# Kernel tuning notes

Measured on AMD Instinct MI355X. Metric: run time of the kernel, lower is better.

The kernel has to match this reference:

```python
import jax, jax.numpy as jnp
import numpy as np

H, I, E, S, K = 768, 3072, 16, 2, 2
SCALE = 1.0  # routed_scaling_factor


def setup_inputs() -> dict:
    key = jax.random.key(0)
    ks = jax.random.split(key, 8)
    sd = 0.02
    return {
        "hidden_states": jax.random.normal(ks[0], (2, 1024, H), jnp.float32),
        "gate_w": jax.random.normal(ks[1], (E, H), jnp.float32) * sd,   # router nn.Linear(H,E).weight
        "shared_wg": jax.random.normal(ks[2], (S, H, I), jnp.float32) * sd,
        "shared_wu": jax.random.normal(ks[3], (S, H, I), jnp.float32) * sd,
        "shared_wd": jax.random.normal(ks[4], (S, I, H), jnp.float32) * sd,
        "wg": jax.random.normal(ks[5], (E, H, I), jnp.float32) * sd,
        "wu": jax.random.normal(ks[6], (E, H, I), jnp.float32) * sd,
        "wd": jax.random.normal(ks[7], (E, I, H), jnp.float32) * sd,
    }


def reference(hidden_states, gate_w, shared_wg, shared_wu, shared_wd, wg, wu, wd):
    B, T, _ = hidden_states.shape
    x = hidden_states.reshape(-1, H)                       # [N, H], N = B*T
    N = x.shape[0]

    # ---- shared experts: always-on, averaged ----
    g = jnp.einsum('nh,shi->sni', x, shared_wg)
    u = jnp.einsum('nh,shi->sni', x, shared_wu)
    shared_out = jnp.einsum('sni,sih->snh', jax.nn.silu(g) * u, shared_wd).mean(axis=0)

    # ---- router: softmax scores, top-k, renormalize, scale ----
    router_logits = x @ gate_w.T                           # [N, E]
    routing_weights = jax.nn.softmax(router_logits, axis=-1)
    topk_w, topk_idx = jax.lax.top_k(routing_weights, K)   # [N, K]
    topk_w = topk_w / (topk_w.sum(axis=-1, keepdims=True) + 1e-8)
    topk_w = topk_w * SCALE

    # combine weights: [N, E], zero for non-selected experts (duplicates summed,
    # matching the torch per-token weight-sum semantics)
    combine = jnp.zeros((N, E), x.dtype).at[jnp.arange(N)[:, None], topk_idx].add(topk_w)

    # ---- routed experts: weighted combine (w=0 for unselected -> same math) ----
    ge = jnp.einsum('nh,ehi->eni', x, wg)                  # [E, N, I]
    ue = jnp.einsum('nh,ehi->eni', x, wu)
    ye = jnp.einsum('eni,eih->enh', jax.nn.silu(ge) * ue, wd)  # [E, N, H]
    routed_out = jnp.einsum('ne,enh->nh', combine, ye)

    return (shared_out + routed_out).reshape(B, T, H)
```

## Files before the change

### kernel.cpp

```cpp
#include <hip/hip_runtime.h>
#include <hip/hip_bf16.h>

#define H 768
#define I_DIM 3072
#define NEXP 16
#define TOPK 2

typedef __bf16 bf16;
typedef __bf16 bf16x8 __attribute__((ext_vector_type(8)));
typedef float f32x4 __attribute__((ext_vector_type(4)));

__device__ __forceinline__ int swizzle_mtile(int bx, int gx) {
    int per = gx >> 3;
    if ((per << 3) != gx) return bx;
    return (bx & 7) * per + (bx >> 3);
}

__global__ void cvt_x_kernel(const float* __restrict__ x, bf16* __restrict__ xb, int n) {
    int i = (blockIdx.x * blockDim.x + threadIdx.x) * 8;
    if (i >= n) return;
    f32x4 v0 = *(const f32x4*)(x + i);
    f32x4 v1 = *(const f32x4*)(x + i + 4);
    bf16x8 p;
#pragma unroll
    for (int j = 0; j < 4; j++) { p[j] = (bf16)v0[j]; p[4 + j] = (bf16)v1[j]; }
    *(bf16x8*)(xb + i) = p;
}

__global__ void router_kernel(const float* __restrict__ x, const float* __restrict__ gw,
                              int* __restrict__ tk_e, float* __restrict__ tk_w,
                              int* __restrict__ counts, int N) {
    int wave = threadIdx.x >> 6;
    int lane = threadIdx.x & 63;
    int t = blockIdx.x * 4 + wave;
    if (t >= N) return;
    const float* xr = x + (size_t)t * H;
    float acc[NEXP];
#pragma unroll
    for (int e = 0; e < NEXP; e++) acc[e] = 0.f;
    for (int h0 = 0; h0 < H; h0 += 64) {
        float xv = xr[h0 + lane];
#pragma unroll
        for (int e = 0; e < NEXP; e++) acc[e] += xv * gw[e * H + h0 + lane];
    }
#pragma unroll
    for (int e = 0; e < NEXP; e++) {
#pragma unroll
        for (int off = 32; off > 0; off >>= 1) acc[e] += __shfl_xor(acc[e], off);
    }
    if (lane == 0) {
        float m = acc[0];
#pragma unroll
        for (int e = 1; e < NEXP; e++) m = fmaxf(m, acc[e]);
        float p[NEXP]; float z = 0.f;
#pragma unroll
        for (int e = 0; e < NEXP; e++) { p[e] = expf(acc[e] - m); z += p[e]; }
        float inv = 1.f / z;
#pragma unroll
        for (int e = 0; e < NEXP; e++) p[e] *= inv;
        int i0 = 0; float v0 = p[0];
#pragma unroll
        for (int e = 1; e < NEXP; e++) if (p[e] > v0) { v0 = p[e]; i0 = e; }
        int i1 = -1; float v1 = -1.f;
#pragma unroll
        for (int e = 0; e < NEXP; e++) if (e != i0 && p[e] > v1) { v1 = p[e]; i1 = e; }
        float s = 1.f / (v0 + v1 + 1e-8f);
        tk_e[t * 2 + 0] = i0; tk_w[t * 2 + 0] = v0 * s;
        tk_e[t * 2 + 1] = i1; tk_w[t * 2 + 1] = v1 * s;
        atomicAdd(&counts[i0], 1);
        atomicAdd(&counts[i1], 1);
    }
}

__global__ void scan_fill_kernel(const int* __restrict__ counts, int* __restrict__ cursors,
                                 int* __restrict__ pad_off, int* __restrict__ rows_token,
                                 float* __restrict__ rows_weight, int N) {
    __shared__ int s_total;
    if (threadIdx.x == 0) {
        int off = 0;
        for (int e = 0; e < NEXP; e++) {
            pad_off[e] = off;
            cursors[e] = off;
            off += (counts[e] + 127) & ~127;
        }
        pad_off[NEXP] = off;
        s_total = off;
    }
    __syncthreads();
    int total = s_total;
    for (int r = threadIdx.x; r < 2 * N; r += blockDim.x) {
        rows_token[r] = r & (N - 1);
        rows_weight[r] = 0.5f;
    }
    for (int r = threadIdx.x; r < total; r += blockDim.x) {
        rows_token[2 * N + r] = 0;
        rows_weight[2 * N + r] = 0.f;
    }
}

__global__ void scatter_kernel(const int* __restrict__ tk_e, const float* __restrict__ tk_w,
                               int* __restrict__ cursors, int* __restrict__ rows_token,
                               float* __restrict__ rows_weight, int N) {
    int i = blockIdx.x * blockDim.x + threadIdx.x;
    if (i >= N * TOPK) return;
    int e = tk_e[i];
    int pos = atomicAdd(&cursors[e], 1);
    rows_token[2 * N + pos] = i >> 1;
    rows_weight[2 * N + pos] = tk_w[i];
}

__global__ __launch_bounds__(256) void phaseA_kernel(
        const bf16* __restrict__ xb, const float* __restrict__ swg, const float* __restrict__ swu,
        const float* __restrict__ wg, const float* __restrict__ wu,
        const int* __restrict__ pad_off, const int* __restrict__ rows_token,
        bf16* __restrict__ P, int N, int ic0, int ichunk) {
    int mtile = swizzle_mtile(blockIdx.x, gridDim.x);
    int ntile = blockIdx.y;
    int sh_tiles = (2 * N) / 128;
    int rowbase; const float* gptr; const float* uptr;
    if (mtile < sh_tiles) {
        rowbase = mtile * 128;
        int s = rowbase / N;
        gptr = swg + (size_t)s * H * I_DIM;
        uptr = swu + (size_t)s * H * I_DIM;
    } else {
        int rm = (mtile - sh_tiles) * 128;
        if (rm >= pad_off[NEXP]) return;
        int e = NEXP - 1;
        for (int q = 0; q < NEXP; q++) { if (rm < pad_off[q + 1]) { e = q; break; } }
        rowbase = 2 * N + rm;
        gptr = wg + (size_t)e * H * I_DIM;
        uptr = wu + (size_t)e * H * I_DIM;
    }
    int icol0 = ic0 + ntile * 64;
    int pcol0 = ntile * 64;

    __shared__ bf16 As[2][128][40];
    __shared__ bf16 Bgs[2][64][40];
    __shared__ bf16 Bus[2][64][40];
    __shared__ int sTok[128];

    int tid = threadIdx.x;
    if (tid < 128) sTok[tid] = rows_token[rowbase + tid];
    __syncthreads();

    f32x4 accG[4][2], accU[4][2];
#pragma unroll
    for (int i = 0; i < 4; i++)
#pragma unroll
        for (int j = 0; j < 2; j++) {
            accG[i][j] = (f32x4){0.f, 0.f, 0.f, 0.f};
            accU[i][j] = (f32x4){0.f, 0.f, 0.f, 0.f};
        }

    int ar = tid >> 1, ah = tid & 1;
    const bf16* arow = xb + (size_t)sTok[ar] * H + ah * 16;
    int bn = tid & 63, bkq = tid >> 6;
    const float* gbase = gptr + icol0 + bn;
    const float* ubase = uptr + icol0 + bn;

    int lane = tid & 63, w = tid >> 6;
    int wm = (w & 1) * 64, wn = (w >> 1) * 32;
    int fr = lane & 15, fq = (lane >> 4) * 8;

    bf16x8 rA0, rA1;
    float gv[8], uv[8];

#define PA_LOADK(kk)                                                          \
    {                                                                         \
        rA0 = *(const bf16x8*)(arow + (kk));                                  \
        rA1 = *(const bf16x8*)(arow + (kk) + 8);                              \
        _Pragma("unroll")                                                     \
        for (int j = 0; j < 8; j++) {                                         \
            gv[j] = gbase[(size_t)((kk) + bkq * 8 + j) * I_DIM];              \
            uv[j] = ubase[(size_t)((kk) + bkq * 8 + j) * I_DIM];              \
        }                                                                     \
    }
#define PA_STORE(buf)                                                         \
    {                                                                         \
        *(bf16x8*)&As[buf][ar][ah * 16] = rA0;                                \
        *(bf16x8*)&As[buf][ar][ah * 16 + 8] = rA1;                            \
        bf16x8 pg, pu;                                                        \
        _Pragma("unroll")                                                     \
        for (int j = 0; j < 8; j++) { pg[j] = (bf16)gv[j]; pu[j] = (bf16)uv[j]; } \
        *(bf16x8*)&Bgs[buf][bn][bkq * 8] = pg;                                \
        *(bf16x8*)&Bus[buf][bn][bkq * 8] = pu;                                \
    }

    PA_LOADK(0);
    PA_STORE(0);
    __syncthreads();

#pragma unroll
    for (int kb = 0; kb < 24; kb++) {
        if (kb < 23) PA_LOADK((kb + 1) * 32);
        int cur = kb & 1;
        bf16x8 a[4], bg[2], bu[2];
#pragma unroll
        for (int mi = 0; mi < 4; mi++) a[mi] = *(const bf16x8*)&As[cur][wm + mi * 16 + fr][fq];
#pragma unroll
        for (int ni = 0; ni < 2; ni++) {
            bg[ni] = *(const bf16x8*)&Bgs[cur][wn + ni * 16 + fr][fq];
            bu[ni] = *(const bf16x8*)&Bus[cur][wn + ni * 16 + fr][fq];
        }
#pragma unroll
        for (int mi = 0; mi < 4; mi++)
#pragma unroll
            for (int ni = 0; ni < 2; ni++) {
                accG[mi][ni] = __builtin_amdgcn_mfma_f32_16x16x32_bf16(a[mi], bg[ni], accG[mi][ni], 0, 0, 0);
                accU[mi][ni] = __builtin_amdgcn_mfma_f32_16x16x32_bf16(a[mi], bu[ni], accU[mi][ni], 0, 0, 0);
            }
        if (kb < 23) {
            PA_STORE(cur ^ 1);
            __syncthreads();
        }
    }

    int cq = lane >> 4;
#pragma unroll
    for (int mi = 0; mi < 4; mi++)
#pragma unroll
        for (int ni = 0; ni < 2; ni++) {
            int n = wn + ni * 16 + fr;
#pragma unroll
            for (int rr = 0; rr < 4; rr++) {
                int m = wm + mi * 16 + cq * 4 + rr;
                float g = accG[mi][ni][rr];
                float u = accU[mi][ni][rr];
                float pv = (g / (1.f + __expf(-g))) * u;
                P[(size_t)(rowbase + m) * ichunk + pcol0 + n] = (bf16)pv;
            }
        }
}

__global__ __launch_bounds__(256) void phaseB_kernel(
        const bf16* __restrict__ P, const float* __restrict__ swd, const float* __restrict__ wd,
        const int* __restrict__ pad_off, const int* __restrict__ rows_token,
        const float* __restrict__ rows_weight, float* __restrict__ out,
        int N, int ic0, int ichunk) {
    int mtile = swizzle_mtile(blockIdx.x, gridDim.x);
    int ntile = blockIdx.y;
    int sh_tiles = (2 * N) / 128;
    int rowbase; const float* dptr;
    if (mtile < sh_tiles) {
        rowbase = mtile * 128;
        int s = rowbase / N;
        dptr = swd + (size_t)s * I_DIM * H;
    } else {
        int rm = (mtile - sh_tiles) * 128;
        if (rm >= pad_off[NEXP]) return;
        int e = NEXP - 1;
        for (int q = 0; q < NEXP; q++) { if (rm < pad_off[q + 1]) { e = q; break; } }
        rowbase = 2 * N + rm;
        dptr = wd + (size_t)e * I_DIM * H;
    }
    int h0 = ntile * 128;

    __shared__ bf16 As[2][128][40];
    __shared__ bf16 Bs[2][128][40];
    __shared__ int sTok[128];
    __shared__ float sW[128];

    int tid = threadIdx.x;
    if (tid < 128) {
        sTok[tid] = rows_token[rowbase + tid];
        sW[tid] = rows_weight[rowbase + tid];
    }
    __syncthreads();

    f32x4 acc[4][4];
#pragma unroll
    for (int i = 0; i < 4; i++)
#pragma unroll
        for (int j = 0; j < 4; j++) acc[i][j] = (f32x4){0.f, 0.f, 0.f, 0.f};

    int ar = tid >> 1, ah = tid & 1;
    const bf16* arow = P + (size_t)(rowbase + ar) * ichunk + ah * 16;
    int bcol = tid & 127, bko = (tid >> 7) * 16;
    const float* dbase = dptr + (size_t)ic0 * H + h0 + bcol;

    int lane = tid & 63, w = tid >> 6;
    int wm = (w & 1) * 64, wn = (w >> 1) * 64;
    int fr = lane & 15, fq = (lane >> 4) * 8;

    bf16x8 rA0, rA1;
    float dv[16];

#define PB_LOADK(kk)                                                          \
    {                                                                         \
        rA0 = *(const bf16x8*)(arow + (kk));                                  \
        rA1 = *(const bf16x8*)(arow + (kk) + 8);                              \
        _Pragma("unroll")                                                     \
        for (int j = 0; j < 16; j++)                                          \
            dv[j] = dbase[(size_t)((kk) + bko + j) * H];                      \
    }
#define PB_STORE(buf)                                                         \
    {                                                                         \
        *(bf16x8*)&As[buf][ar][ah * 16] = rA0;                                \
        *(bf16x8*)&As[buf][ar][ah * 16 + 8] = rA1;                            \
        bf16x8 p0, p1;                                                        \
        _Pragma("unroll")                                                     \
        for (int j = 0; j < 8; j++) { p0[j] = (bf16)dv[j]; p1[j] = (bf16)dv[8 + j]; } \
        *(bf16x8*)&Bs[buf][bcol][bko] = p0;                                   \
        *(bf16x8*)&Bs[buf][bcol][bko + 8] = p1;                               \
    }

    PB_LOADK(0);
    PB_STORE(0);
    __syncthreads();

    int KB = ichunk >> 5;
    for (int kb = 0; kb < KB; kb++) {
        if (kb + 1 < KB) PB_LOADK((kb + 1) * 32);
        int cur = kb & 1;
        bf16x8 a[4], b[4];
#pragma unroll
        for (int mi = 0; mi < 4; mi++) a[mi] = *(const bf16x8*)&As[cur][wm + mi * 16 + fr][fq];
#pragma unroll
        for (int ni = 0; ni < 4; ni++) b[ni] = *(const bf16x8*)&Bs[cur][wn + ni * 16 + fr][fq];
#pragma unroll
        for (int mi = 0; mi < 4; mi++)
#pragma unroll
            for (int ni = 0; ni < 4; ni++)
                acc[mi][ni] = __builtin_amdgcn_mfma_f32_16x16x32_bf16(a[mi], b[ni], acc[mi][ni], 0, 0, 0);
        if (kb + 1 < KB) {
            PB_STORE(cur ^ 1);
            __syncthreads();
        }
    }

    int cq = lane >> 4;
#pragma unroll
    for (int mi = 0; mi < 4; mi++)
#pragma unroll
        for (int ni = 0; ni < 4; ni++) {
            int n = wn + ni * 16 + fr;
#pragma unroll
            for (int rr = 0; rr < 4; rr++) {
                int m = wm + mi * 16 + cq * 4 + rr;
                atomicAdd(&out[(size_t)sTok[m] * H + h0 + n], sW[m] * acc[mi][ni][rr]);
            }
        }
}

extern "C" void kernel_launch(void* const* d_in, const int* in_sizes, int n_in,
                              void* d_out, int out_size, void* d_ws, size_t ws_size,
                              hipStream_t stream) {
    const float* x   = (const float*)d_in[0];
    const float* gw  = (const float*)d_in[1];
    const float* swg = (const float*)d_in[2];
    const float* swu = (const float*)d_in[3];
    const float* swd = (const float*)d_in[4];
    const float* wg  = (const float*)d_in[5];
    const float* wu  = (const float*)d_in[6];
    const float* wd  = (const float*)d_in[7];
    float* out = (float*)d_out;

    int N = in_sizes[0] / H;
    int ROWCAP = 2 * N + N * TOPK + NEXP * 128;

    int* wsi = (int*)d_ws;
    int* counts     = wsi + 0;
    int* cursors    = wsi + 16;
    int* pad_off    = wsi + 32;
    int* tk_e       = wsi + 64;
    float* tk_w     = (float*)(wsi + 64 + 2 * N);
    int* rows_token = wsi + 64 + 4 * N;
    float* rows_weight = (float*)(wsi + 64 + 4 * N + ROWCAP);

    size_t xb_off = 131072;
    bf16* xb = (bf16*)((char*)d_ws + xb_off);
    size_t pbase = xb_off + (size_t)N * H * 2;

    const int cand[10] = {3072, 1536, 1024, 768, 512, 384, 256, 192, 128, 64};
    int ichunk = 64;
    for (int i = 0; i < 10; i++) {
        if (pbase + (size_t)ROWCAP * cand[i] * 2 <= ws_size) { ichunk = cand[i]; break; }
    }
    bf16* P = (bf16*)((char*)d_ws + pbase);

    hipMemsetAsync(d_out, 0, (size_t)out_size * sizeof(float), stream);
    hipMemsetAsync(d_ws, 0, 256, stream);

    cvt_x_kernel<<<(N * H) / 2048, 256, 0, stream>>>(x, xb, N * H);
    router_kernel<<<(N + 3) / 4, 256, 0, stream>>>(x, gw, tk_e, tk_w, counts, N);
    scan_fill_kernel<<<1, 256, 0, stream>>>(counts, cursors, pad_off, rows_token, rows_weight, N);
    scatter_kernel<<<(N * TOPK + 255) / 256, 256, 0, stream>>>(tk_e, tk_w, cursors, rows_token, rows_weight, N);

    int sh_tiles = (2 * N) / 128;
    int rt_tiles = (N * TOPK + NEXP * 128) / 128;
    for (int ic0 = 0; ic0 < I_DIM; ic0 += ichunk) {
        dim3 gA(sh_tiles + rt_tiles, ichunk / 64);
        phaseA_kernel<<<gA, dim3(256), 0, stream>>>(xb, swg, swu, wg, wu, pad_off, rows_token, P, N, ic0, ichunk);
        dim3 gB(sh_tiles + rt_tiles, H / 128);
        phaseB_kernel<<<gB, dim3(256), 0, stream>>>(P, swd, wd, pad_off, rows_token, rows_weight, out, N, ic0, ichunk);
    }
}
```

Before: 840.3 us.

## Pre-transpose and convert expert weights to bf16 K-major before GEMMs

Adds a transpose+convert kernel that writes all shared and routed gate/up/down weights into bf16 K-contiguous layouts in workspace, followed by new phase A/B GEMM kernels that read those bf16 transposed weights with vectorized loads. The goal is to halve weight bandwidth and avoid in-kernel fp32 conversion and strided weight access. The cost is a full pass over roughly 340MB of fp32 weights on every call plus extra workspace, with a fallback to the old path when the workspace is too small.

Result: slower. 880.8 us (+4.8%).

```diff
diff --git a/kernel.cpp b/kernel.cpp
--- a/kernel.cpp
+++ b/kernel.cpp
@@ -7,6 +7,7 @@
 #define TOPK 2
 
 typedef __bf16 bf16;
+typedef __bf16 bf16x4 __attribute__((ext_vector_type(4)));
 typedef __bf16 bf16x8 __attribute__((ext_vector_type(8)));
 typedef float f32x4 __attribute__((ext_vector_type(4)));
 
@@ -25,6 +26,32 @@
 #pragma unroll
     for (int j = 0; j < 4; j++) { p[j] = (bf16)v0[j]; p[4 + j] = (bf16)v1[j]; }
     *(bf16x8*)(xb + i) = p;
+}
+
+__global__ __launch_bounds__(256) void transpose_cvt_kernel(
+        const float* __restrict__ in, bf16* __restrict__ outp, int R, int C) {
+    __shared__ bf16 t[64][74];
+    const float* ip = in + (size_t)blockIdx.z * R * C;
+    bf16* op = outp + (size_t)blockIdx.z * R * C;
+    int c0 = blockIdx.x * 64, r0 = blockIdx.y * 64;
+    int tid = threadIdx.x;
+    int lr = tid >> 4, lc = (tid & 15) * 4;
+#pragma unroll
+    for (int p = 0; p < 4; p++) {
+        int r = p * 16 + lr;
+        f32x4 v = *(const f32x4*)(ip + (size_t)(r0 + r) * C + (c0 + lc));
+        bf16x4 b;
+#pragma unroll
+        for (int j = 0; j < 4; j++) b[j] = (bf16)v[j];
+        *(bf16x4*)&t[r][lc] = b;
+    }
+    __syncthreads();
+    int oc = tid >> 2, s = (tid & 3) * 16;
+    bf16x8 o0, o1;
+#pragma unroll
+    for (int j = 0; j < 8; j++) { o0[j] = t[s + j][oc]; o1[j] = t[s + 8 + j][oc]; }
+    *(bf16x8*)(op + (size_t)(c0 + oc) * R + (r0 + s)) = o0;
+    *(bf16x8*)(op + (size_t)(c0 + oc) * R + (r0 + s + 8)) = o1;
 }
 
 __global__ void router_kernel(const float* __restrict__ x, const float* __restrict__ gw,
@@ -107,6 +134,227 @@
     int pos = atomicAdd(&cursors[e], 1);
     rows_token[2 * N + pos] = i >> 1;
     rows_weight[2 * N + pos] = tk_w[i];
+}
+
+__global__ __launch_bounds__(256) void phaseA_t_kernel(
+        const bf16* __restrict__ xb, const bf16* __restrict__ WgT, const bf16* __restrict__ WuT,
+        const int* __restrict__ pad_off, const int* __restrict__ rows_token,
+        bf16* __restrict__ P, int N, int ic0, int ichunk) {
+    int mtile = swizzle_mtile(blockIdx.x, gridDim.x);
+    int ntile = blockIdx.y;
+    int sh_tiles = (2 * N) / 128;
+    int rowbase; const bf16* gptr; const bf16* uptr;
+    if (mtile < sh_tiles) {
+        rowbase = mtile * 128;
+        int s = rowbase / N;
+        gptr = WgT + (size_t)s * I_DIM * H;
+        uptr = WuT + (size_t)s * I_DIM * H;
+    } else {
+        int rm = (mtile - sh_tiles) * 128;
+        if (rm >= pad_off[NEXP]) return;
+        int e = NEXP - 1;
+        for (int q = 0; q < NEXP; q++) { if (rm < pad_off[q + 1]) { e = q; break; } }
+        rowbase = 2 * N + rm;
+        gptr = WgT + (size_t)(2 + e) * I_DIM * H;
+        uptr = WuT + (size_t)(2 + e) * I_DIM * H;
+    }
+    int icol0 = ic0 + ntile * 64;
+    int pcol0 = ntile * 64;
+
+    __shared__ bf16 As[2][128][40];
+    __shared__ bf16 Bgs[2][64][40];
+    __shared__ bf16 Bus[2][64][40];
+    __shared__ int sTok[128];
+
+    int tid = threadIdx.x;
+    if (tid < 128) sTok[tid] = rows_token[rowbase + tid];
+    __syncthreads();
+
+    f32x4 accG[4][2], accU[4][2];
+#pragma unroll
+    for (int i = 0; i < 4; i++)
+#pragma unroll
+        for (int j = 0; j < 2; j++) {
+            accG[i][j] = (f32x4){0.f, 0.f, 0.f, 0.f};
+            accU[i][j] = (f32x4){0.f, 0.f, 0.f, 0.f};
+        }
+
+    int ar = tid >> 1, ah = tid & 1;
+    const bf16* arow = xb + (size_t)sTok[ar] * H + ah * 16;
+    int bn = tid >> 2, bkq = tid & 3;
+    const bf16* gb = gptr + (size_t)(icol0 + bn) * H + bkq * 8;
+    const bf16* ub = uptr + (size_t)(icol0 + bn) * H + bkq * 8;
+
+    int lane = tid & 63, w = tid >> 6;
+    int wm = (w & 1) * 64, wn = (w >> 1) * 32;
+    int fr = lane & 15, fq = (lane >> 4) * 8;
+
+    bf16x8 rA0, rA1, rG, rU;
+
+#define PAT_LOADK(kk)                                                         \
+    {                                                                         \
+        rA0 = *(const bf16x8*)(arow + (kk));                                  \
+        rA1 = *(const bf16x8*)(arow + (kk) + 8);                              \
+        rG = *(const bf16x8*)(gb + (kk));                                     \
+        rU = *(const bf16x8*)(ub + (kk));                                     \
+    }
+#define PAT_STORE(buf)                                                        \
+    {                                                                         \
+        *(bf16x8*)&As[buf][ar][ah * 16] = rA0;                                \
+        *(bf16x8*)&As[buf][ar][ah * 16 + 8] = rA1;                            \
+        *(bf16x8*)&Bgs[buf][bn][bkq * 8] = rG;                                \
+        *(bf16x8*)&Bus[buf][bn][bkq * 8] = rU;                                \
+    }
+
+    PAT_LOADK(0);
+    PAT_STORE(0);
+    __syncthreads();
+
+#pragma unroll
+    for (int kb = 0; kb < 24; kb++) {
+        if (kb < 23) PAT_LOADK((kb + 1) * 32);
+        int cur = kb & 1;
+        bf16x8 a[4], bg[2], bu[2];
+#pragma unroll
+        for (int mi = 0; mi < 4; mi++) a[mi] = *(const bf16x8*)&As[cur][wm + mi * 16 + fr][fq];
+#pragma unroll
+        for (int ni = 0; ni < 2; ni++) {
+            bg[ni] = *(const bf16x8*)&Bgs[cur][wn + ni * 16 + fr][fq];
+            bu[ni] = *(const bf16x8*)&Bus[cur][wn + ni * 16 + fr][fq];
+        }
+#pragma unroll
+        for (int mi = 0; mi < 4; mi++)
+#pragma unroll
+            for (int ni = 0; ni < 2; ni++) {
+                accG[mi][ni] = __builtin_amdgcn_mfma_f32_16x16x32_bf16(a[mi], bg[ni], accG[mi][ni], 0, 0, 0);
+                accU[mi][ni] = __builtin_amdgcn_mfma_f32_16x16x32_bf16(a[mi], bu[ni], accU[mi][ni], 0, 0, 0);
+            }
+        if (kb < 23) {
+            PAT_STORE(cur ^ 1);
+            __syncthreads();
+        }
+    }
+
+    int cq = lane >> 4;
+#pragma unroll
+    for (int mi = 0; mi < 4; mi++)
+#pragma unroll
+        for (int ni = 0; ni < 2; ni++) {
+            int n = wn + ni * 16 + fr;
+#pragma unroll
+            for (int rr = 0; rr < 4; rr++) {
+                int m = wm + mi * 16 + cq * 4 + rr;
+                float g = accG[mi][ni][rr];
+                float u = accU[mi][ni][rr];
+                float pv = (g / (1.f + __expf(-g))) * u;
+                P[(size_t)(rowbase + m) * ichunk + pcol0 + n] = (bf16)pv;
+            }
+        }
+}
+
+__global__ __launch_bounds__(256) void phaseB_t_kernel(
+        const bf16* __restrict__ P, const bf16* __restrict__ WdT,
+        const int* __restrict__ pad_off, const int* __restrict__ rows_token,
+        const float* __restrict__ rows_weight, float* __restrict__ out,
+        int N, int ic0, int ichunk) {
+    int mtile = swizzle_mtile(blockIdx.x, gridDim.x);
+    int ntile = blockIdx.y;
+    int sh_tiles = (2 * N) / 128;
+    int rowbase; const bf16* dptr;
+    if (mtile < sh_tiles) {
+        rowbase = mtile * 128;
+        int s = rowbase / N;
+        dptr = WdT + (size_t)s * I_DIM * H;
+    } else {
+        int rm = (mtile - sh_tiles) * 128;
+        if (rm >= pad_off[NEXP]) return;
+        int e = NEXP - 1;
+        for (int q = 0; q < NEXP; q++) { if (rm < pad_off[q + 1]) { e = q; break; } }
+        rowbase = 2 * N + rm;
+        dptr = WdT + (size_t)(2 + e) * I_DIM * H;
+    }
+    int h0 = ntile * 128;
+
+    __shared__ bf16 As[2][128][40];
+    __shared__ bf16 Bs[2][128][40];
+    __shared__ int sTok[128];
+    __shared__ float sW[128];
+
+    int tid = threadIdx.x;
+    if (tid < 128) {
+        sTok[tid] = rows_token[rowbase + tid];
+        sW[tid] = rows_weight[rowbase + tid];
+    }
+    __syncthreads();
+
+    f32x4 acc[4][4];
+#pragma unroll
+    for (int i = 0; i < 4; i++)
+#pragma unroll
+        for (int j = 0; j < 4; j++) acc[i][j] = (f32x4){0.f, 0.f, 0.f, 0.f};
+
+    int ar = tid >> 1, ah = tid & 1;
+    const bf16* arow = P + (size_t)(rowbase + ar) * ichunk + ah * 16;
+    int bn = tid >> 1, bkh = tid & 1;
+    const bf16* db = dptr + (size_t)(h0 + bn) * I_DIM + ic0 + bkh * 16;
+
+    int lane = tid & 63, w = tid >> 6;
+    int wm = (w & 1) * 64, wn = (w >> 1) * 64;
+    int fr = lane & 15, fq = (lane >> 4) * 8;
+
+    bf16x8 rA0, rA1, rB0, rB1;
+
+#define PBT_LOADK(kk)                                                         \
+    {                                                                         \
+        rA0 = *(const bf16x8*)(arow + (kk));                                  \
+        rA1 = *(const bf16x8*)(arow + (kk) + 8);                              \
+        rB0 = *(const bf16x8*)(db + (kk));                                    \
+        rB1 = *(const bf16x8*)(db + (kk) + 8);                                \
+    }
+#define PBT_STORE(buf)                                                        \
+    {                                                                         \
+        *(bf16x8*)&As[buf][ar][ah * 16] = rA0;                                \
+        *(bf16x8*)&As[buf][ar][ah * 16 + 8] = rA1;                            \
+        *(bf16x8*)&Bs[buf][bn][bkh * 16] = rB0;                               \
+        *(bf16x8*)&Bs[buf][bn][bkh * 16 + 8] = rB1;                           \
+    }
+
+    PBT_LOADK(0);
+    PBT_STORE(0);
+    __syncthreads();
+
+    int KB = ichunk >> 5;
+    for (int kb = 0; kb < KB; kb++) {
+        if (kb + 1 < KB) PBT_LOADK((kb + 1) * 32);
+        int cur = kb & 1;
+        bf16x8 a[4], b[4];
+#pragma unroll
+        for (int mi = 0; mi < 4; mi++) a[mi] = *(const bf16x8*)&As[cur][wm + mi * 16 + fr][fq];
+#pragma unroll
+        for (int ni = 0; ni < 4; ni++) b[ni] = *(const bf16x8*)&Bs[cur][wn + ni * 16 + fr][fq];
+#pragma unroll
+        for (int mi = 0; mi < 4; mi++)
+#pragma unroll
+            for (int ni = 0; ni < 4; ni++)
+                acc[mi][ni] = __builtin_amdgcn_mfma_f32_16x16x32_bf16(a[mi], b[ni], acc[mi][ni], 0, 0, 0);
+        if (kb + 1 < KB) {
+            PBT_STORE(cur ^ 1);
+            __syncthreads();
+        }
+    }
+
+    int cq = lane >> 4;
+#pragma unroll
+    for (int mi = 0; mi < 4; mi++)
+#pragma unroll
+        for (int ni = 0; ni < 4; ni++) {
+            int n = wn + ni * 16 + fr;
+#pragma unroll
+            for (int rr = 0; rr < 4; rr++) {
+                int m = wm + mi * 16 + cq * 4 + rr;
+                atomicAdd(&out[(size_t)sTok[m] * H + h0 + n], sW[m] * acc[mi][ni][rr]);
+            }
+        }
 }
 
 __global__ __launch_bounds__(256) void phaseA_kernel(
@@ -373,11 +621,15 @@
     size_t pbase = xb_off + (size_t)N * H * 2;
 
     const int cand[10] = {3072, 1536, 1024, 768, 512, 384, 256, 192, 128, 64};
-    int ichunk = 64;
+
+    size_t MATEL = (size_t)I_DIM * H;
+    size_t WB = 18 * MATEL * 2;
+    size_t wt_off = pbase;
+    size_t p2base = wt_off + 3 * WB;
+    int ichunk2 = 0;
     for (int i = 0; i < 10; i++) {
-        if (pbase + (size_t)ROWCAP * cand[i] * 2 <= ws_size) { ichunk = cand[i]; break; }
-    }
-    bf16* P = (bf16*)((char*)d_ws + pbase);
+        if (p2base + (size_t)ROWCAP * cand[i] * 2 <= ws_size) { ichunk2 = cand[i]; break; }
+    }
 
     hipMemsetAsync(d_out, 0, (size_t)out_size * sizeof(float), stream);
     hipMemsetAsync(d_ws, 0, 256, stream);
@@ -389,10 +641,38 @@
 
     int sh_tiles = (2 * N) / 128;
     int rt_tiles = (N * TOPK + NEXP * 128) / 128;
-    for (int ic0 = 0; ic0 < I_DIM; ic0 += ichunk) {
-        dim3 gA(sh_tiles + rt_tiles, ichunk / 64);
-        phaseA_kernel<<<gA, dim3(256), 0, stream>>>(xb, swg, swu, wg, wu, pad_off, rows_token, P, N, ic0, ichunk);
-        dim3 gB(sh_tiles + rt_tiles, H / 128);
-        phaseB_kernel<<<gB, dim3(256), 0, stream>>>(P, swd, wd, pad_off, rows_token, rows_weight, out, N, ic0, ichunk);
-    }
-}
+
+    if (ichunk2 > 0) {
+        bf16* WgT = (bf16*)((char*)d_ws + wt_off);
+        bf16* WuT = WgT + 18 * MATEL;
+        bf16* WdT = WuT + 18 * MATEL;
+        bf16* P = (bf16*)((char*)d_ws + p2base);
+        int ichunk = ichunk2;
+
+        transpose_cvt_kernel<<<dim3(I_DIM / 64, H / 64, 2), 256, 0, stream>>>(swg, WgT, H, I_DIM);
+        transpose_cvt_kernel<<<dim3(I_DIM / 64, H / 64, 16), 256, 0, stream>>>(wg, WgT + 2 * MATEL, H, I_DIM);
+        transpose_cvt_kernel<<<dim3(I_DIM / 64, H / 64, 2), 256, 0, stream>>>(swu, WuT, H, I_DIM);
+        transpose_cvt_kernel<<<dim3(I_DIM / 64, H / 64, 16), 256, 0, stream>>>(wu, WuT + 2 * MATEL, H, I_DIM);
+        transpose_cvt_kernel<<<dim3(H / 64, I_DIM / 64, 2), 256, 0, stream>>>(swd, WdT, I_DIM, H);
+        transpose_cvt_kernel<<<dim3(H / 64, I_DIM / 64, 16), 256, 0, stream>>>(wd, WdT + 2 * MATEL, I_DIM, H);
+
+        for (int ic0 = 0; ic0 < I_DIM; ic0 += ichunk) {
+            dim3 gA(sh_tiles + rt_tiles, ichunk / 64);
+            phaseA_t_kernel<<<gA, dim3(256), 0, stream>>>(xb, WgT, WuT, pad_off, rows_token, P, N, ic0, ichunk);
+            dim3 gB(sh_tiles + rt_tiles, H / 128);
+            phaseB_t_kernel<<<gB, dim3(256), 0, stream>>>(P, WdT, pad_off, rows_token, rows_weight, out, N, ic0, ichunk);
+        }
+    } else {
+        int ichunk = 64;
+        for (int i = 0; i < 10; i++) {
+            if (pbase + (size_t)ROWCAP * cand[i] * 2 <= ws_size) { ichunk = cand[i]; break; }
+        }
+        bf16* P = (bf16*)((char*)d_ws + pbase);
+        for (int ic0 = 0; ic0 < I_DIM; ic0 += ichunk) {
+            dim3 gA(sh_tiles + rt_tiles, ichunk / 64);
+            phaseA_kernel<<<gA, dim3(256), 0, stream>>>(xb, swg, swu, wg, wu, pad_off, rows_token, P, N, ic0, ichunk);
+            dim3 gB(sh_tiles + rt_tiles, H / 128);
+            phaseB_kernel<<<gB, dim3(256), 0, stream>>>(P, swd, wd, pad_off, rows_token, rows_weight, out, N, ic0, ichunk);
+        }
+    }
+}
```
